# Kernel tuning notes

Hardware: AMD Instinct MI355X
Metric: run time of the kernel (lower is better)

## Reference

```python
import jax, jax.numpy as jnp
import numpy as np
import math

D_MODEL = 512
N_HEADS = 8
D_FF = 2048
TOP_FACTOR = 5
LN_EPS = 1e-5


def _layernorm(x, g, b):
    m = jnp.mean(x, axis=-1, keepdims=True)
    v = jnp.mean((x - m) ** 2, axis=-1, keepdims=True)
    return (x - m) / jnp.sqrt(v + LN_EPS) * g + b


def _prob_sparse_attn(q_in, k_in, v_in, wq, bq, wk, bk, wv, bv, wo, bo):
    # weights stored (in, out): y = x @ w + b  (equivalent to torch Linear)
    B, Lq, dm = q_in.shape
    Lk = k_in.shape[1]
    H, D = N_HEADS, dm // N_HEADS
    q = (q_in @ wq + bq).reshape(B, Lq, H, D).transpose(0, 2, 1, 3)  # (B,H,Lq,D)
    k = (k_in @ wk + bk).reshape(B, Lk, H, D).transpose(0, 2, 1, 3)
    v = (v_in @ wv + bv).reshape(B, Lk, H, D).transpose(0, 2, 1, 3)

    qn = q / jnp.linalg.norm(q, axis=-1, keepdims=True)
    kn = k / jnp.linalg.norm(k, axis=-1, keepdims=True)
    # full cosine-similarity matrix, reduced to a row mean (as in the original)
    scores_all = jnp.einsum('bhqd,bhkd->bhqk', qn, kn)
    mean_scores = scores_all.mean(axis=-1)  # (B,H,Lq)

    u = max(1, Lq // TOP_FACTOR)
    _, top_idx = jax.lax.top_k(mean_scores, u)  # (B,H,u)

    q_sel = jnp.take_along_axis(q, top_idx[..., None], axis=2)  # (B,H,u,D)
    scores = jnp.einsum('bhud,bhkd->bhuk', q_sel, k) / math.sqrt(D)
    attn = jax.nn.softmax(scores, axis=-1)
    ctx_sel = jnp.einsum('bhuk,bhkd->bhud', attn, v)  # (B,H,u,D)

    b_ix = jnp.arange(B)[:, None, None]
    h_ix = jnp.arange(H)[None, :, None]
    context = jnp.zeros((B, H, Lq, D), dtype=q.dtype).at[b_ix, h_ix, top_idx].set(ctx_sel)
    out = context.transpose(0, 2, 1, 3).reshape(B, Lq, dm)
    return out @ wo + bo


def _decoder_layer(x, enc_out, p):
    xn = _layernorm(x, p['ln1_g'], p['ln1_b'])
    x = x + _prob_sparse_attn(xn, xn, xn, p['sa_wq'], p['sa_bq'], p['sa_wk'], p['sa_bk'],
                              p['sa_wv'], p['sa_bv'], p['sa_wo'], p['sa_bo'])
    xn = _layernorm(x, p['ln2_g'], p['ln2_b'])
    x = x + _prob_sparse_attn(xn, enc_out, enc_out, p['ca_wq'], p['ca_bq'], p['ca_wk'], p['ca_bk'],
                              p['ca_wv'], p['ca_bv'], p['ca_wo'], p['ca_bo'])
    xn = _layernorm(x, p['ln3_g'], p['ln3_b'])
    h = jax.nn.relu(xn @ p['ff_w1'] + p['ff_b1'])
    return x + (h @ p['ff_w2'] + p['ff_b2'])


def setup_inputs() -> dict:
    key = jax.random.key(0)
    ks = iter(jax.random.split(key, 32))
    B, L = 2, 2048
    dm, dff = D_MODEL, D_FF
    s = 1.0 / math.sqrt(dm)
    inp = {
        'x': jax.random.normal(next(ks), (B, L, dm), jnp.float32),
        'enc_out': jax.random.normal(next(ks), (B, L, dm), jnp.float32),
    }
    for pre in ('sa', 'ca'):
        for nm in ('wq', 'wk', 'wv', 'wo'):
            inp[f'{pre}_{nm}'] = jax.random.normal(next(ks), (dm, dm), jnp.float32) * s
            inp[f'{pre}_{nm[1:] and "b" + nm[1:]}'] = jnp.zeros((dm,), jnp.float32)
    inp['ff_w1'] = jax.random.normal(next(ks), (dm, dff), jnp.float32) * s
    inp['ff_b1'] = jnp.zeros((dff,), jnp.float32)
    inp['ff_w2'] = jax.random.normal(next(ks), (dff, dm), jnp.float32) / math.sqrt(dff)
    inp['ff_b2'] = jnp.zeros((dm,), jnp.float32)
    for i in (1, 2, 3):
        inp[f'ln{i}_g'] = jnp.ones((dm,), jnp.float32)
        inp[f'ln{i}_b'] = jnp.zeros((dm,), jnp.float32)
    return inp


def reference(x, enc_out,
              sa_wq, sa_bq, sa_wk, sa_bk, sa_wv, sa_bv, sa_wo, sa_bo,
              ca_wq, ca_bq, ca_wk, ca_bk, ca_wv, ca_bv, ca_wo, ca_bo,
              ff_w1, ff_b1, ff_w2, ff_b2,
              ln1_g, ln1_b, ln2_g, ln2_b, ln3_g, ln3_b):
    p = dict(sa_wq=sa_wq, sa_bq=sa_bq, sa_wk=sa_wk, sa_bk=sa_bk, sa_wv=sa_wv, sa_bv=sa_bv,
             sa_wo=sa_wo, sa_bo=sa_bo, ca_wq=ca_wq, ca_bq=ca_bq, ca_wk=ca_wk, ca_bk=ca_bk,
             ca_wv=ca_wv, ca_bv=ca_bv, ca_wo=ca_wo, ca_bo=ca_bo,
             ff_w1=ff_w1, ff_b1=ff_b1, ff_w2=ff_w2, ff_b2=ff_b2,
             ln1_g=ln1_g, ln1_b=ln1_b, ln2_g=ln2_g, ln2_b=ln2_b, ln3_g=ln3_g, ln3_b=ln3_b)
    return _decoder_layer(x, enc_out, p)
```

## Files before the change

### kernel.cpp

```cpp
#include <hip/hip_runtime.h>

#define BB 2
#define LL 2048
#define DM 512
#define NH 8
#define DH 64
#define DFF 2048
#define UU 409
#define ROWS (BB*LL)
#define X_ELEMS 2097152
#define NCHUNK 8

typedef unsigned short u16;
typedef __attribute__((ext_vector_type(8))) short short8;
typedef __attribute__((ext_vector_type(4))) float floatx4;

#define G_TOTAL 38200000
__device__ float g_buf[G_TOTAL];
__device__ int   g_isbf16;

#define A_Q     10495488
#define A_K     12592640
#define A_V     14689792
#define A_MKN   25175552
#define A_MS    25176576
#define A_RANK  25209344
#define A_PARTK 25242112
#define A_LIST  25274880
#define A_PO    25281536
#define A_PML   29475840
#define A_CTXF  16786944
#define XN_H    16796672
#define XN_L    18893824
#define CTX_H   33573888
#define CTX_L   35671040
#define ENC_H   37768192
#define ENC_L   39865344
#define AH_H    41962496
#define KH16    59213824
#define KL16    61310976
#define VTH16   63408128
#define VTL16   65505280
#define WT_SAQKV 67864576
#define WT_SAO   69437440
#define WT_CAQ   69961728
#define WT_CAKV  70486016
#define WT_CAO   71534592
#define WT_W1    72058880
#define WT_W2    74156032

__constant__ int c_end[28] = {
    2097152, 4194304, 4456448, 4456960, 4719104, 4719616, 4981760, 4982272,
    5244416, 5244928, 5507072, 5507584, 5769728, 5770240, 6032384, 6032896,
    6295040, 6295552, 7344128, 7346176, 8394752, 8395264, 8395776, 8396288,
    8396800, 8397312, 8397824, 8398336
};
__constant__ int sm_idx[16] = {3,5,7,9,11,13,15,17,19,21,22,23,24,25,26,27};
__constant__ int sm_cum[16] = {64,128,192,256,320,384,448,512,768,832,896,960,1024,1088,1152,1216};
#define XG 262144
#define EG 262144
#define SG 1216

__device__ __forceinline__ float bf2f(u16 x) {
    union { unsigned int u; float f; } c; c.u = ((unsigned int)x) << 16; return c.f;
}
__device__ __forceinline__ u16 f2bf(float f) {
    union { float f; unsigned int u; } c; c.f = f;
    unsigned int u = c.u;
    return (u16)((u + 0x7FFFu + ((u >> 16) & 1u)) >> 16);
}
__device__ __forceinline__ unsigned cvtpk_bf16(float a, float b) {
    unsigned r;
    asm("v_cvt_pk_bf16_f32 %0, %1, %2" : "=v"(r) : "v"(a), "v"(b));
    return r;
}

struct P28 { const void* p[28]; };
struct I3 { int v[3]; };

__constant__ int tj[10][6] = {
    {2,  WT_SAQKV, 0,    512,  786432, 8},
    {4,  WT_SAQKV, 512,  512,  786432, 8},
    {6,  WT_SAQKV, 1024, 512,  786432, 8},
    {8,  WT_SAO,   0,    512,  262144, 8},
    {10, WT_CAQ,   0,    512,  262144, 8},
    {12, WT_CAKV,  0,    512,  524288, 8},
    {14, WT_CAKV,  512,  512,  524288, 8},
    {16, WT_CAO,   0,    512,  262144, 8},
    {18, WT_W1,    0,    512, 1048576, 32},
    {20, WT_W2,    0,   2048, 1048576, 8},
};
__constant__ int tcum[10] = {64, 128, 192, 256, 320, 384, 448, 512, 768, 1024};
__global__ void prep_all(P28 ps) {
    const int f = (((const u16*)ps.p[22])[0] == 0x3F80u) ? 1 : 0;
    if (blockIdx.x == 0 && threadIdx.x == 0) g_isbf16 = f;
    u16* gb16 = (u16*)g_buf;
    if (blockIdx.x < 1024) {
        int bid = blockIdx.x;
        int j = 0;
        while (bid >= tcum[j]) j++;
        int t = bid - (j ? tcum[j - 1] : 0);
        int widx = tj[j][0], wt = tj[j][1], col0 = tj[j][2];
        int K = tj[j][3], lo = tj[j][4], txn = tj[j][5];
        int Nsrc = txn * 64;
        int n0 = (t % txn) * 64, k0 = (t / txn) * 64;
        __shared__ float tb[64][65];
        int c = threadIdx.x & 63, r0 = threadIdx.x >> 6;
        const void* W = ps.p[widx];
        u16* WTh = gb16 + wt;
        for (int i = 0; i < 16; i++) {
            int r = r0 + 4 * i;
            size_t src = (size_t)(k0 + r) * Nsrc + n0 + c;
            tb[r][c] = f ? bf2f(((const u16*)W)[src]) : ((const float*)W)[src];
        }
        __syncthreads();
        for (int i = 0; i < 16; i++) {
            int r = r0 + 4 * i;
            float v = tb[c][r];
            u16 hi = f2bf(v);
            size_t o = (size_t)(col0 + n0 + r) * K + k0 + c;
            WTh[o] = hi;
            WTh[lo + o] = f2bf(v - bf2f(hi));
        }
        return;
    }
    int stride = 2048 * blockDim.x;
    for (int g = (blockIdx.x - 1024) * blockDim.x + threadIdx.x; g < XG + EG + SG; g += stride) {
        if (g < XG) {
            int e = g * 8;
            if (f) {
                uint4 raw = ((const uint4*)ps.p[0])[g];
                const u16* rr = (const u16*)&raw;
                float v[8] __attribute__((aligned(16)));
#pragma unroll
                for (int i = 0; i < 8; i++) v[i] = bf2f(rr[i]);
                *(float4*)(g_buf + e) = ((const float4*)v)[0];
                *(float4*)(g_buf + e + 4) = ((const float4*)v)[1];
            } else {
                *(uint4*)(g_buf + e)     = ((const uint4*)ps.p[0])[g * 2];
                *(uint4*)(g_buf + e + 4) = ((const uint4*)ps.p[0])[g * 2 + 1];
            }
        } else if (g < XG + EG) {
            int gl = g - XG;
            int e = gl * 8;
            float v[8] __attribute__((aligned(16)));
            if (f) {
                uint4 raw = ((const uint4*)ps.p[1])[gl];
                const u16* rr = (const u16*)&raw;
#pragma unroll
                for (int i = 0; i < 8; i++) v[i] = bf2f(rr[i]);
            } else {
                *(float4*)(v)     = ((const float4*)ps.p[1])[gl * 2];
                *(float4*)(v + 4) = ((const float4*)ps.p[1])[gl * 2 + 1];
            }
            u16 hh[8] __attribute__((aligned(16)));
            u16 lo[8] __attribute__((aligned(16)));
#pragma unroll
            for (int i = 0; i < 8; i++) { u16 hi = f2bf(v[i]); hh[i] = hi; lo[i] = f2bf(v[i] - bf2f(hi)); }
            *(uint4*)(&gb16[ENC_H + e]) = *(const uint4*)hh;
            *(uint4*)(&gb16[ENC_L + e]) = *(const uint4*)lo;
        } else {
            int t = g - XG - EG;
            int si = 0;
            while (t >= sm_cum[si]) si++;
            int s = sm_idx[si];
            int gl = t - (si ? sm_cum[si - 1] : 0);
            int e = gl * 8;
            float* dst = g_buf + c_end[s - 1] + e;
            if (f) {
                uint4 raw = *(const uint4*)((const u16*)ps.p[s] + e);
                const u16* rr = (const u16*)&raw;
#pragma unroll
                for (int i = 0; i < 8; i++) dst[i] = bf2f(rr[i]);
            } else {
                *(uint4*)(dst)     = *(const uint4*)((const float*)ps.p[s] + e);
                *(uint4*)(dst + 4) = *(const uint4*)((const float*)ps.p[s] + e + 4);
            }
        }
    }
}

__global__ void lnorm_k(int x_off, int g_off, int b_off, int yh_u16, int yl_u16) {
    int row = blockIdx.x;
    int tid = threadIdx.x;
    const float* x = g_buf + x_off + (size_t)row * DM;
    float a = x[tid], c = x[tid + 256];
    float s1 = a + c, s2 = a * a + c * c;
    for (int o = 32; o > 0; o >>= 1) { s1 += __shfl_xor(s1, o); s2 += __shfl_xor(s2, o); }
    __shared__ float r1[4], r2[4];
    int wave = tid >> 6, lane = tid & 63;
    if (lane == 0) { r1[wave] = s1; r2[wave] = s2; }
    __syncthreads();
    s1 = r1[0] + r1[1] + r1[2] + r1[3];
    s2 = r2[0] + r2[1] + r2[2] + r2[3];
    float mean = s1 * (1.0f / DM);
    float var  = s2 * (1.0f / DM) - mean * mean;
    float rstd = rsqrtf(var + 1e-5f);
    const float* gg = g_buf + g_off;
    const float* bb = g_buf + b_off;
    u16* yh = ((u16*)g_buf) + yh_u16 + (size_t)row * DM;
    u16* yl = ((u16*)g_buf) + yl_u16 + (size_t)row * DM;
    float v1 = (a - mean) * rstd * gg[tid]       + bb[tid];
    float v2 = (c - mean) * rstd * gg[tid + 256] + bb[tid + 256];
    u16 h1 = f2bf(v1), h2 = f2bf(v2);
    yh[tid] = h1;       yl[tid] = f2bf(v1 - bf2f(h1));
    yh[tid + 256] = h2; yl[tid + 256] = f2bf(v2 - bf2f(h2));
}

template<int WM, bool SPLIT, bool SEC, bool RELU, bool RESID, bool FINAL, bool OUTH>
__global__ void mgemm_k(I3 a_offs, I3 splt, I3 alz, int wt_u16_off, I3 boffs, int resid_off,
                        int out_off, void* __restrict__ dext, int M, int N, int K) {
    constexpr int BT_M = WM * 32;
    constexpr int A4 = BT_M * 4;
    __shared__ u16 Ash[BT_M * 40];
    __shared__ u16 Asl[SPLIT ? BT_M * 40 : 8];
    __shared__ u16 Bsh[128 * 40];
    __shared__ u16 Bsl[SPLIT ? 128 * 40 : 8];
    int ntb = blockIdx.y;
    int sec_blk = SEC ? ((ntb * 128) >> 9) : 0;
    const u16* Ah = ((const u16*)g_buf) + a_offs.v[sec_blk];
    const u16* Al = Ah + (size_t)M * K;
    const u16* WTh = ((const u16*)g_buf) + wt_u16_off;
    const u16* WTl = WTh + (size_t)N * K;
    const int isbf = g_isbf16;
    const bool use_al = SPLIT && splt.v[sec_blk] && !(alz.v[sec_blk] && isbf);
    const bool use_bl = SPLIT && splt.v[sec_blk] && !isbf;
    int tid = threadIdx.x;
    int lane = tid & 63, wid = tid >> 6;
    int wm = wid >> 1, wn = wid & 1;
    int quad = lane >> 4, l15 = lane & 15;
    int m0 = blockIdx.x * BT_M, n0 = ntb * 128;
    floatx4 acc[WM][4];
#pragma unroll
    for (int i = 0; i < WM; i++)
#pragma unroll
        for (int j = 0; j < 4; j++) acc[i][j] = (floatx4){0.f, 0.f, 0.f, 0.f};
    for (int k0 = 0; k0 < K; k0 += 32) {
#pragma unroll
        for (int i = 0; i < (A4 + 255) / 256; i++) {
            int idx8 = tid + 256 * i;
            if (A4 % 256 == 0 || idx8 < A4) {
                int r = idx8 >> 2, c8 = (idx8 & 3) * 8;
                *(uint4*)(&Ash[r * 40 + c8]) = *(const uint4*)(Ah + (size_t)(m0 + r) * K + k0 + c8);
                if (SPLIT && use_al)
                    *(uint4*)(&Asl[r * 40 + c8]) = *(const uint4*)(Al + (size_t)(m0 + r) * K + k0 + c8);
            }
        }
#pragma unroll
        for (int i = 0; i < 2; i++) {
            int idx8 = tid + 256 * i;
            int r = idx8 >> 2, c8 = (idx8 & 3) * 8;
            *(uint4*)(&Bsh[r * 40 + c8]) = *(const uint4*)(WTh + (size_t)(n0 + r) * K + k0 + c8);
            if (SPLIT && use_bl)
                *(uint4*)(&Bsl[r * 40 + c8]) = *(const uint4*)(WTl + (size_t)(n0 + r) * K + k0 + c8);
        }
        __syncthreads();
        short8 ah[WM], bh[4], al[WM], bl[4];
#pragma unroll
        for (int i = 0; i < WM; i++) {
            int ro = (wm * WM * 16 + i * 16 + l15) * 40 + quad * 8;
            ah[i] = *(const short8*)(&Ash[ro]);
            if (SPLIT && use_al) al[i] = *(const short8*)(&Asl[ro]);
        }
#pragma unroll
        for (int j = 0; j < 4; j++) {
            int ro = (wn * 64 + j * 16 + l15) * 40 + quad * 8;
            bh[j] = *(const short8*)(&Bsh[ro]);
            if (SPLIT && use_bl) bl[j] = *(const short8*)(&Bsl[ro]);
        }
#pragma unroll
        for (int i = 0; i < WM; i++)
#pragma unroll
            for (int j = 0; j < 4; j++) {
                acc[i][j] = __builtin_amdgcn_mfma_f32_16x16x32_bf16(ah[i], bh[j], acc[i][j], 0, 0, 0);
                if constexpr (SPLIT) {
                    if (use_bl)
                        acc[i][j] = __builtin_amdgcn_mfma_f32_16x16x32_bf16(ah[i], bl[j], acc[i][j], 0, 0, 0);
                    if (use_al)
                        acc[i][j] = __builtin_amdgcn_mfma_f32_16x16x32_bf16(al[i], bh[j], acc[i][j], 0, 0, 0);
                }
            }
        __syncthreads();
    }
#pragma unroll
    for (int i = 0; i < WM; i++)
#pragma unroll
        for (int j = 0; j < 4; j++)
#pragma unroll
            for (int r = 0; r < 4; r++) {
                int row = m0 + wm * WM * 16 + i * 16 + quad * 4 + r;
                int col = n0 + wn * 64 + j * 16 + l15;
                int sec = SEC ? (col >> 9) : 0;
                int ci  = SEC ? (col & 511) : col;
                float v = acc[i][j][r] + g_buf[boffs.v[sec] + ci];
                if (RELU) v = fmaxf(v, 0.f);
                if (RESID) v += g_buf[resid_off + (size_t)row * N + col];
                if (FINAL) {
                    if (g_isbf16) ((u16*)dext)[(size_t)row * N + col] = f2bf(v);
                    else          ((float*)dext)[(size_t)row * N + col] = v;
                } else if (OUTH) {
                    ((u16*)g_buf)[out_off + (size_t)row * N + col] = f2bf(v);
                } else if (SEC) {
                    g_buf[out_off + ((size_t)sec * ROWS + row) * 512 + ci] = v;
                } else {
                    g_buf[out_off + (size_t)row * N + col] = v;
                }
            }
}

template<bool SPLIT, bool RESID, bool FINAL>
__global__ __launch_bounds__(64) void sgemm_k(int a_off, int sp, int alz, int wt_u16_off,
        int b_off, int resid_off, int out_off, void* __restrict__ dext, int M, int N, int K) {
    const u16* gb = (const u16*)g_buf;
    const u16* Ah = gb + a_off;
    const u16* Alp = Ah + (size_t)M * K;
    const u16* Bh = gb + wt_u16_off;
    const u16* Blp = Bh + (size_t)N * K;
    const int isbf = g_isbf16;
    const bool ual = SPLIT && sp && !(alz && isbf);
    const bool ubl = SPLIT && sp && !isbf;
    int mtiles = M >> 4;
    int bid = blockIdx.x;
    int mt = bid % mtiles, nt = bid / mtiles;
    int n0 = nt * 64, m0 = mt * 16;
    int lane = threadIdx.x;
    int quad = lane >> 4, l15 = lane & 15;
    const u16* ap  = Ah  + (size_t)(m0 + l15) * K + quad * 8;
    const u16* alq = Alp + (size_t)(m0 + l15) * K + quad * 8;
    const u16* bp  = Bh  + (size_t)(n0 + l15) * K + quad * 8;
    const u16* blq = Blp + (size_t)(n0 + l15) * K + quad * 8;
    floatx4 acc[4];
#pragma unroll
    for (int j = 0; j < 4; j++) acc[j] = (floatx4){0.f, 0.f, 0.f, 0.f};

    short8 AH0, AH1, AH2, AH3, AL0, AL1, AL2, AL3;
    short8 BH0[4], BH1[4], BH2[4], BH3[4], BL0[4], BL1[4], BL2[4], BL3[4];

#define SLOAD(P, KK) do { int kk_ = (KK); \
        AH##P = *(const short8*)(ap + kk_); \
        if (ual) AL##P = *(const short8*)(alq + kk_); \
        _Pragma("unroll") \
        for (int j = 0; j < 4; j++) { \
            BH##P[j] = *(const short8*)(bp + (size_t)j * 16 * K + kk_); \
            if (ubl) BL##P[j] = *(const short8*)(blq + (size_t)j * 16 * K + kk_); \
        } } while (0)

#define SMFMA(P) do { \
        _Pragma("unroll") \
        for (int j = 0; j < 4; j++) { \
            acc[j] = __builtin_amdgcn_mfma_f32_16x16x32_bf16(AH##P, BH##P[j], acc[j], 0, 0, 0); \
            if (SPLIT) { \
                if (ubl) acc[j] = __builtin_amdgcn_mfma_f32_16x16x32_bf16(AH##P, BL##P[j], acc[j], 0, 0, 0); \
                if (ual) acc[j] = __builtin_amdgcn_mfma_f32_16x16x32_bf16(AL##P, BH##P[j], acc[j], 0, 0, 0); \
            } \
        } } while (0)

    SLOAD(0, 0); SLOAD(1, 32); SLOAD(2, 64); SLOAD(3, 96);
    int k0 = 0;
    for (; k0 + 128 < K; k0 += 128) {
        SMFMA(0); SLOAD(0, k0 + 128);
        SMFMA(1); SLOAD(1, k0 + 160);
        SMFMA(2); SLOAD(2, k0 + 192);
        SMFMA(3); SLOAD(3, k0 + 224);
    }
    SMFMA(0); SMFMA(1); SMFMA(2); SMFMA(3);
#undef SLOAD
#undef SMFMA

    const float* bias = g_buf + b_off;
#pragma unroll
    for (int j = 0; j < 4; j++)
#pragma unroll
        for (int r = 0; r < 4; r++) {
            int row = m0 + quad * 4 + r;
            int col = n0 + j * 16 + l15;
            float v = acc[j][r] + bias[col];
            if (RESID) v += g_buf[resid_off + (size_t)row * N + col];
            if (FINAL) {
                if (isbf) ((u16*)dext)[(size_t)row * N + col] = f2bf(v);
                else      ((float*)dext)[(size_t)row * N + col] = v;
            } else {
                g_buf[out_off + (size_t)row * N + col] = v;
            }
        }
}

__global__ void meankn_p1(int k_off, int part_off) {
    int bh = blockIdx.x >> 5, chunk = blockIdx.x & 31;
    int b = bh >> 3, h = bh & 7;
    int wave = threadIdx.x >> 6, lane = threadIdx.x & 63;
    const float* base = g_buf + k_off + (size_t)b * LL * DM + (size_t)h * DH + lane;
    float acc = 0.f;
    for (int t = 0; t < 16; t++) {
        int j = chunk * 64 + wave * 16 + t;
        float kv = base[(size_t)j * DM];
        float s = kv * kv;
        for (int o = 32; o > 0; o >>= 1) s += __shfl_xor(s, o);
        acc += kv / sqrtf(fmaxf(s, 1e-30f));
    }
    __shared__ float red[4][64];
    red[wave][lane] = acc;
    __syncthreads();
    if (threadIdx.x < 64)
        g_buf[part_off + (size_t)blockIdx.x * 64 + threadIdx.x] =
            red[0][threadIdx.x] + red[1][threadIdx.x] + red[2][threadIdx.x] + red[3][threadIdx.x];
}

__global__ void mscore_k(int q_off, int part_off, int ms_off) {
    int bh = blockIdx.y, b = bh >> 3, h = bh & 7;
    int tid = threadIdx.x;
    __shared__ float mk[64];
    if (tid < 64) {
        float s = 0.f;
        for (int c = 0; c < 32; c++) s += g_buf[part_off + (size_t)(bh * 32 + c) * 64 + tid];
        mk[tid] = s * (1.0f / LL);
    }
    __syncthreads();
    int w = tid >> 6, lane = tid & 63;
    float m = mk[lane];
#pragma unroll
    for (int it = 0; it < 8; it++) {
        int row = blockIdx.x * 32 + it * 4 + w;
        float qv = g_buf[q_off + ((size_t)b * LL + row) * DM + h * DH + lane];
        float s = qv * qv, d = qv * m;
        for (int o = 32; o > 0; o >>= 1) { s += __shfl_xor(s, o); d += __shfl_xor(d, o); }
        if (lane == 0) g_buf[ms_off + bh * LL + row] = d / sqrtf(fmaxf(s, 1e-30f));
    }
}

__global__ void topsel_k(int ms_off, int list_off, int rank_off, int u) {
    __shared__ float s[LL];
    int bh = blockIdx.y, chunk = blockIdx.x;
    for (int i = threadIdx.x; i < LL; i += 256) s[i] = g_buf[ms_off + bh * LL + i];
    __syncthreads();
    int il = threadIdx.x >> 2;
    int i = chunk * 64 + il;
    int jq = threadIdx.x & 3;
    float si = s[i];
    int cnt = 0;
    for (int t = 0; t < 512; t++) {
        int j = jq * 512 + t;
        float sj = s[j];
        cnt += (sj > si) || (sj == si && j < i);
    }
    cnt += __shfl_xor(cnt, 1);
    cnt += __shfl_xor(cnt, 2);
    if (jq == 0) {
        int* list = (int*)(g_buf + list_off);
        int* rank = (int*)(g_buf + rank_off);
        if (cnt < u) { list[bh * 416 + cnt] = i; rank[bh * LL + i] = cnt; }
        else rank[bh * LL + i] = -1;
    }
}

template<bool LO>
__global__ void kvprep_k(int k_off, int v_off) {
    int bh = blockIdx.y, b = bh >> 3, h = bh & 7;
    int tok0 = blockIdx.x * 64;
    int tid = threadIdx.x;
    __shared__ float vt[64][68];
    u16* gb16 = (u16*)g_buf;
    int tok = tid >> 2, dq = (tid & 3) * 16;
    const float* kp = g_buf + k_off + ((size_t)(b * LL + tok0 + tok)) * DM + h * DH + dq;
    const float* vp = g_buf + v_off + ((size_t)(b * LL + tok0 + tok)) * DM + h * DH + dq;
    float kv[16] __attribute__((aligned(16)));
#pragma unroll
    for (int i = 0; i < 4; i++) *(float4*)(kv + 4 * i) = *(const float4*)(kp + 4 * i);
    u16 hh[16] __attribute__((aligned(16)));
    u16 lo[16] __attribute__((aligned(16)));
#pragma unroll
    for (int i = 0; i < 16; i++) { hh[i] = f2bf(kv[i]); if (LO) lo[i] = f2bf(kv[i] - bf2f(hh[i])); }
    size_t ko = ((size_t)(bh * LL + tok0 + tok)) * DH + dq;
    *(uint4*)(gb16 + KH16 + ko)     = ((const uint4*)hh)[0];
    *(uint4*)(gb16 + KH16 + ko + 8) = ((const uint4*)hh)[1];
    if (LO) {
        *(uint4*)(gb16 + KL16 + ko)     = ((const uint4*)lo)[0];
        *(uint4*)(gb16 + KL16 + ko + 8) = ((const uint4*)lo)[1];
    }
#pragma unroll
    for (int i = 0; i < 4; i++) *(float4*)(&vt[tok][dq + 4 * i]) = *(const float4*)(vp + 4 * i);
    __syncthreads();
    int d = tid >> 2, tq = (tid & 3) * 16;
    float vv[16];
#pragma unroll
    for (int i = 0; i < 16; i++) vv[i] = vt[tq + i][d];
#pragma unroll
    for (int i = 0; i < 16; i++) { hh[i] = f2bf(vv[i]); if (LO) lo[i] = f2bf(vv[i] - bf2f(hh[i])); }
    size_t vo = ((size_t)(bh * DH + d)) * LL + tok0 + tq;
    *(uint4*)(gb16 + VTH16 + vo)     = ((const uint4*)hh)[0];
    *(uint4*)(gb16 + VTH16 + vo + 8) = ((const uint4*)hh)[1];
    if (LO) {
        *(uint4*)(gb16 + VTL16 + vo)     = ((const uint4*)lo)[0];
        *(uint4*)(gb16 + VTL16 + vo + 8) = ((const uint4*)lo)[1];
    }
}

template<bool S3>
__global__ __launch_bounds__(256, 4) void attn_flash(int q_off, int kh_off, int kl_off,
        int vth_off, int vtl_off, int list_off, int po_off, int pml_off, int u) {
    int bid = blockIdx.x;
    int grp = bid & 127;
    int sxt = bid >> 7;
    int bh = grp & 15, chunk = grp >> 4;
    int b = bh >> 3, h = bh & 7;
    int tid = threadIdx.x, lane = tid & 63, w = tid >> 6;
    int quad = lane >> 4, l15 = lane & 15;
    const int* list = (const int*)(g_buf + list_off);

    short8 qh[2], ql[2];
    {
        int slot_q = sxt * 64 + w * 16 + l15;
        int qidx = list[bh * 416 + (slot_q < u ? slot_q : u - 1)];
        const float* qp = g_buf + q_off + ((size_t)b * LL + qidx) * DM + h * DH;
#pragma unroll
        for (int d2 = 0; d2 < 2; d2++) {
            float v[8] __attribute__((aligned(16)));
            *(float4*)(v)     = *(const float4*)(qp + d2 * 32 + quad * 8);
            *(float4*)(v + 4) = *(const float4*)(qp + d2 * 32 + quad * 8 + 4);
            u16 hh[8] __attribute__((aligned(16)));
            u16 lo[8] __attribute__((aligned(16)));
#pragma unroll
            for (int j = 0; j < 8; j++) {
                float s = v[j] * 0.125f;
                u16 hi = f2bf(s); hh[j] = hi; lo[j] = f2bf(s - bf2f(hi));
            }
            qh[d2] = *(const short8*)hh; ql[d2] = *(const short8*)lo;
        }
    }

    __shared__ u16 Ksh[32 * 68];
    __shared__ u16 Ksl[S3 ? 32 * 68 : 8];
    __shared__ u16 Vth[64 * 36];
    __shared__ u16 Vtl[S3 ? 64 * 36 : 8];

    const u16* gb16 = (const u16*)g_buf;
    const u16* KHp = gb16 + kh_off + (size_t)bh * LL * DH;
    const u16* KLp = gb16 + kl_off + (size_t)bh * LL * DH;
    const u16* VHp = gb16 + vth_off + (size_t)bh * DH * LL;
    const u16* VLp = gb16 + vtl_off + (size_t)bh * DH * LL;
    int krow = tid >> 3, kcol = (tid & 7) * 8;
    int vd = tid >> 2, vcol = (tid & 3) * 8;

    int aA = ((((lane >> 4) & 1) << 5) | l15) << 2;
    int aB = aA + 64;
    bool hiT = (quad >= 2);

    uint4 pre[S3 ? 4 : 2];
    auto issue = [&](int row0) {
        pre[0] = *(const uint4*)(KHp + (size_t)(row0 + krow) * DH + kcol);
        pre[1] = *(const uint4*)(VHp + (size_t)vd * LL + row0 + vcol);
        if constexpr (S3) {
            pre[2] = *(const uint4*)(KLp + (size_t)(row0 + krow) * DH + kcol);
            pre[3] = *(const uint4*)(VLp + (size_t)vd * LL + row0 + vcol);
        }
    };
    auto commit = [&]() {
        *(uint4*)(&Ksh[krow * 68 + kcol]) = pre[0];
        *(uint4*)(&Vth[vd * 36 + vcol]) = pre[1];
        if constexpr (S3) {
            *(uint4*)(&Ksl[krow * 68 + kcol]) = pre[2];
            *(uint4*)(&Vtl[vd * 36 + vcol]) = pre[3];
        }
    };

    float m_run = -3.0e38f, l_run = 0.f;
    floatx4 acc_o[4];
#pragma unroll
    for (int j = 0; j < 4; j++) acc_o[j] = (floatx4){0.f, 0.f, 0.f, 0.f};

    issue(chunk * 256);
    for (int kt = 0; kt < 8; ++kt) {
        __syncthreads();
        commit();
        if (kt < 7) issue(chunk * 256 + (kt + 1) * 32);
        __syncthreads();
        floatx4 sacc[2];
#pragma unroll
        for (int t = 0; t < 2; t++) {
            sacc[t] = (floatx4){0.f, 0.f, 0.f, 0.f};
#pragma unroll
            for (int d2 = 0; d2 < 2; d2++) {
                int ro = (t * 16 + l15) * 68 + d2 * 32 + quad * 8;
                short8 kh = *(const short8*)(&Ksh[ro]);
                sacc[t] = __builtin_amdgcn_mfma_f32_16x16x32_bf16(kh, qh[d2], sacc[t], 0, 0, 0);
                sacc[t] = __builtin_amdgcn_mfma_f32_16x16x32_bf16(kh, ql[d2], sacc[t], 0, 0, 0);
                if constexpr (S3) {
                    short8 kl = *(const short8*)(&Ksl[ro]);
                    sacc[t] = __builtin_amdgcn_mfma_f32_16x16x32_bf16(kl, qh[d2], sacc[t], 0, 0, 0);
                }
            }
        }
        float mx = fmaxf(fmaxf(fmaxf(sacc[0][0], sacc[0][1]), fmaxf(sacc[0][2], sacc[0][3])),
                         fmaxf(fmaxf(sacc[1][0], sacc[1][1]), fmaxf(sacc[1][2], sacc[1][3])));
        mx = fmaxf(mx, __shfl_xor(mx, 16));
        mx = fmaxf(mx, __shfl_xor(mx, 32));
        float mn = fmaxf(m_run, mx);
        float alpha = __expf(m_run - mn);
        m_run = mn;
#pragma unroll
        for (int t = 0; t < 2; t++)
#pragma unroll
            for (int r = 0; r < 4; r++) sacc[t][r] = __expf(sacc[t][r] - mn);
        float ls = (sacc[0][0] + sacc[0][1]) + (sacc[0][2] + sacc[0][3])
                 + (sacc[1][0] + sacc[1][1]) + (sacc[1][2] + sacc[1][3]);
        ls += __shfl_xor(ls, 16);
        ls += __shfl_xor(ls, 32);
        l_run = l_run * alpha + ls;
        unsigned phw[2][2], plw[2][2];
#pragma unroll
        for (int t = 0; t < 2; t++)
#pragma unroll
            for (int hh = 0; hh < 2; hh++) {
                float s0 = sacc[t][2 * hh], s1 = sacc[t][2 * hh + 1];
                unsigned hw = cvtpk_bf16(s0, s1);
                phw[t][hh] = hw;
                float r0 = s0 - __uint_as_float(hw << 16);
                float r1 = s1 - __uint_as_float(hw & 0xFFFF0000u);
                plw[t][hh] = cvtpk_bf16(r0, r1);
            }
        union { unsigned wd[4]; short8 v; } pbh, pbl;
#pragma unroll
        for (int hh = 0; hh < 2; hh++) {
            int a0 = __builtin_amdgcn_ds_bpermute(aA, (int)phw[0][hh]);
            int a1 = __builtin_amdgcn_ds_bpermute(aA, (int)phw[1][hh]);
            pbh.wd[hh] = (unsigned)(hiT ? a1 : a0);
            int b0 = __builtin_amdgcn_ds_bpermute(aB, (int)phw[0][hh]);
            int b1 = __builtin_amdgcn_ds_bpermute(aB, (int)phw[1][hh]);
            pbh.wd[2 + hh] = (unsigned)(hiT ? b1 : b0);
            int c0 = __builtin_amdgcn_ds_bpermute(aA, (int)plw[0][hh]);
            int c1 = __builtin_amdgcn_ds_bpermute(aA, (int)plw[1][hh]);
            pbl.wd[hh] = (unsigned)(hiT ? c1 : c0);
            int d0 = __builtin_amdgcn_ds_bpermute(aB, (int)plw[0][hh]);
            int d1 = __builtin_amdgcn_ds_bpermute(aB, (int)plw[1][hh]);
            pbl.wd[2 + hh] = (unsigned)(hiT ? d1 : d0);
        }
#pragma unroll
        for (int j = 0; j < 4; j++)
#pragma unroll
            for (int r = 0; r < 4; r++) acc_o[j][r] *= alpha;
#pragma unroll
        for (int j = 0; j < 4; j++) {
            int ro = (j * 16 + l15) * 36 + quad * 8;
            short8 vh = *(const short8*)(&Vth[ro]);
            acc_o[j] = __builtin_amdgcn_mfma_f32_16x16x32_bf16(vh, pbh.v, acc_o[j], 0, 0, 0);
            acc_o[j] = __builtin_amdgcn_mfma_f32_16x16x32_bf16(vh, pbl.v, acc_o[j], 0, 0, 0);
            if constexpr (S3) {
                short8 vl = *(const short8*)(&Vtl[ro]);
                acc_o[j] = __builtin_amdgcn_mfma_f32_16x16x32_bf16(vl, pbh.v, acc_o[j], 0, 0, 0);
            }
        }
    }
    int slot = sxt * 64 + w * 16 + l15;
    if (slot < u) {
        size_t rec = ((size_t)(bh * NCHUNK + chunk)) * 512 + slot;
        float* po = g_buf + po_off + rec * 64;
#pragma unroll
        for (int j = 0; j < 4; j++)
            *(float4*)(po + j * 16 + quad * 4) = *(const float4*)&acc_o[j];
        if (quad == 0) {
            float* pml = g_buf + pml_off + rec * 2;
            pml[0] = m_run; pml[1] = l_run;
        }
    }
}

__global__ void attn_combine(int po_off, int pml_off, int rank_off, int u) {
    int bh = blockIdx.y;
    int b = bh >> 3, h = bh & 7;
    int tid = threadIdx.x;
    int qi = tid >> 4;
    int kb = tid & 15;
    int ds = kb * 4;
    int row = blockIdx.x * 16 + qi;
    int rank = ((const int*)(g_buf + rank_off))[bh * LL + row];
    size_t idx = ((size_t)b * LL + row) * DM + h * DH + ds;
    if (rank < 0) {
        ushort4 z = {0, 0, 0, 0};
        *(ushort4*)(((u16*)g_buf) + CTX_H + idx) = z;
        *(ushort4*)(((u16*)g_buf) + CTX_L + idx) = z;
        return;
    }
    float m = -3.0e38f;
#pragma unroll
    for (int c = 0; c < NCHUNK; c++)
        m = fmaxf(m, g_buf[pml_off + (((size_t)(bh * NCHUNK + c)) * 512 + rank) * 2]);
    float l = 0.f, O0 = 0.f, O1 = 0.f, O2 = 0.f, O3 = 0.f;
#pragma unroll
    for (int c = 0; c < NCHUNK; c++) {
        size_t rec = ((size_t)(bh * NCHUNK + c)) * 512 + rank;
        const float* pml = g_buf + pml_off + rec * 2;
        float a = __expf(pml[0] - m);
        l += a * pml[1];
        float4 o = *(const float4*)(g_buf + po_off + rec * 64 + ds);
        O0 += a * o.x; O1 += a * o.y; O2 += a * o.z; O3 += a * o.w;
    }
    float inv = 1.0f / l;
    float o0 = O0 * inv, o1 = O1 * inv, o2 = O2 * inv, o3 = O3 * inv;
    ushort4 hv, lv;
    hv.x = f2bf(o0); lv.x = f2bf(o0 - bf2f(hv.x));
    hv.y = f2bf(o1); lv.y = f2bf(o1 - bf2f(hv.y));
    hv.z = f2bf(o2); lv.z = f2bf(o2 - bf2f(hv.z));
    hv.w = f2bf(o3); lv.w = f2bf(o3 - bf2f(hv.w));
    *(ushort4*)(((u16*)g_buf) + CTX_H + idx) = hv;
    *(ushort4*)(((u16*)g_buf) + CTX_L + idx) = lv;
}

extern "C" void kernel_launch(void* const* d_in, const int* in_sizes, int n_in,
                              void* d_out, int out_size, void* d_ws, size_t ws_size,
                              hipStream_t stream) {
    static const int SZ[28] = {
        2097152, 2097152,
        262144, 512, 262144, 512, 262144, 512, 262144, 512,
        262144, 512, 262144, 512, 262144, 512, 262144, 512,
        1048576, 2048, 1048576, 512,
        512, 512, 512, 512, 512, 512
    };
    int OFF[28];
    int cur = 0;
    for (int i = 0; i < 28; i++) { OFF[i] = cur; cur += SZ[i]; }

    P28 ps;
    for (int i = 0; i < 28; i++) ps.p[i] = d_in[i];
    prep_all<<<3072, 256, 0, stream>>>(ps);

    auto select_attend = [&](bool sa) {
        if (sa) kvprep_k<true><<<dim3(32, 16), 256, 0, stream>>>(A_K, A_V);
        else    kvprep_k<false><<<dim3(32, 16), 256, 0, stream>>>(A_K, A_V);
        meankn_p1<<<16 * 32, 256, 0, stream>>>(A_K, A_PARTK);
        mscore_k<<<dim3(64, 16), 256, 0, stream>>>(A_Q, A_PARTK, A_MS);
        topsel_k<<<dim3(32, 16), 256, 0, stream>>>(A_MS, A_LIST, A_RANK, UU);
        if (sa)
            attn_flash<true><<<896, 256, 0, stream>>>(
                A_Q, KH16, KL16, VTH16, VTL16, A_LIST, A_PO, A_PML, UU);
        else
            attn_flash<false><<<896, 256, 0, stream>>>(
                A_Q, KH16, KL16, VTH16, VTL16, A_LIST, A_PO, A_PML, UU);
        attn_combine<<<dim3(128, 16), 256, 0, stream>>>(A_PO, A_PML, A_RANK, UU);
    };

    lnorm_k<<<ROWS, 256, 0, stream>>>(OFF[0], OFF[22], OFF[23], XN_H, XN_L);
    mgemm_k<2, true, true, false, false, false, false><<<dim3(64, 12), 256, 0, stream>>>(
        I3{{XN_H, XN_H, XN_H}}, I3{{1, 1, 1}}, I3{{0, 0, 0}},
        WT_SAQKV, I3{{OFF[3], OFF[5], OFF[7]}}, 0, A_Q, nullptr, ROWS, 1536, 512);
    select_attend(true);
    sgemm_k<true, true, false><<<2048, 64, 0, stream>>>(
        CTX_H, 1, 0, WT_SAO, OFF[9], OFF[0], OFF[0], nullptr, ROWS, 512, 512);

    lnorm_k<<<ROWS, 256, 0, stream>>>(OFF[0], OFF[24], OFF[25], XN_H, XN_L);
    sgemm_k<true, false, false><<<2048, 64, 0, stream>>>(
        XN_H, 1, 0, WT_CAQ, OFF[11], 0, A_Q, nullptr, ROWS, 512, 512);
    mgemm_k<2, true, true, false, false, false, false><<<dim3(64, 8), 256, 0, stream>>>(
        I3{{ENC_H, ENC_H, ENC_H}}, I3{{1, 0, 0}}, I3{{1, 0, 0}},
        WT_CAKV, I3{{OFF[13], OFF[15], 0}}, 0, A_K, nullptr, ROWS, 1024, 512);
    select_attend(false);
    sgemm_k<false, true, false><<<2048, 64, 0, stream>>>(
        CTX_H, 0, 0, WT_CAO, OFF[17], OFF[0], OFF[0], nullptr, ROWS, 512, 512);

    lnorm_k<<<ROWS, 256, 0, stream>>>(OFF[0], OFF[26], OFF[27], XN_H, XN_L);
    mgemm_k<4, false, false, true, false, false, true><<<dim3(32, 16), 256, 0, stream>>>(
        I3{{XN_H, 0, 0}}, I3{{0, 0, 0}}, I3{{0, 0, 0}},
        WT_W1, I3{{OFF[19], 0, 0}}, 0, AH_H, nullptr, ROWS, 2048, 512);
    sgemm_k<false, true, true><<<2048, 64, 0, stream>>>(
        AH_H, 0, 0, WT_W2, OFF[21], OFF[0], 0, d_out, ROWS, 512, 2048);
}
```

Before: 621.0 us.

## Register-prefetch next K tile in mgemm and add sgemm launch bound hint

The tiled MFMA GEMM now loads the next K-slice from global memory into registers while the current slice is being computed, then writes it to shared memory at the top of the next iteration. This software pipelining is meant to hide global load latency behind the MFMA work, and the trailing barrier moves to the start of the loop. It also adds a min-blocks hint of 2 to the small sgemm kernel's launch bounds. The cost is extra registers for the prefetch buffers, which could reduce occupancy, especially in the split-precision variants.

```diff
diff --git a/kernel.cpp b/kernel.cpp
--- a/kernel.cpp
+++ b/kernel.cpp
@@ -212,6 +212,7 @@
                         int out_off, void* __restrict__ dext, int M, int N, int K) {
     constexpr int BT_M = WM * 32;
     constexpr int A4 = BT_M * 4;
+    constexpr int NA = (A4 + 255) / 256;
     __shared__ u16 Ash[BT_M * 40];
     __shared__ u16 Asl[SPLIT ? BT_M * 40 : 8];
     __shared__ u16 Bsh[128 * 40];
@@ -230,30 +231,58 @@
     int wm = wid >> 1, wn = wid & 1;
     int quad = lane >> 4, l15 = lane & 15;
     int m0 = blockIdx.x * BT_M, n0 = ntb * 128;
-    floatx4 acc[WM][4];
-#pragma unroll
-    for (int i = 0; i < WM; i++)
-#pragma unroll
-        for (int j = 0; j < 4; j++) acc[i][j] = (floatx4){0.f, 0.f, 0.f, 0.f};
-    for (int k0 = 0; k0 < K; k0 += 32) {
-#pragma unroll
-        for (int i = 0; i < (A4 + 255) / 256; i++) {
+
+    uint4 pA[NA], pAl[NA], pB[2], pBl[2];
+    auto issue = [&](int k0) {
+#pragma unroll
+        for (int i = 0; i < NA; i++) {
             int idx8 = tid + 256 * i;
             if (A4 % 256 == 0 || idx8 < A4) {
                 int r = idx8 >> 2, c8 = (idx8 & 3) * 8;
-                *(uint4*)(&Ash[r * 40 + c8]) = *(const uint4*)(Ah + (size_t)(m0 + r) * K + k0 + c8);
+                pA[i] = *(const uint4*)(Ah + (size_t)(m0 + r) * K + k0 + c8);
                 if (SPLIT && use_al)
-                    *(uint4*)(&Asl[r * 40 + c8]) = *(const uint4*)(Al + (size_t)(m0 + r) * K + k0 + c8);
+                    pAl[i] = *(const uint4*)(Al + (size_t)(m0 + r) * K + k0 + c8);
             }
         }
 #pragma unroll
         for (int i = 0; i < 2; i++) {
             int idx8 = tid + 256 * i;
             int r = idx8 >> 2, c8 = (idx8 & 3) * 8;
-            *(uint4*)(&Bsh[r * 40 + c8]) = *(const uint4*)(WTh + (size_t)(n0 + r) * K + k0 + c8);
+            pB[i] = *(const uint4*)(WTh + (size_t)(n0 + r) * K + k0 + c8);
             if (SPLIT && use_bl)
-                *(uint4*)(&Bsl[r * 40 + c8]) = *(const uint4*)(WTl + (size_t)(n0 + r) * K + k0 + c8);
-        }
+                pBl[i] = *(const uint4*)(WTl + (size_t)(n0 + r) * K + k0 + c8);
+        }
+    };
+    auto commit = [&]() {
+#pragma unroll
+        for (int i = 0; i < NA; i++) {
+            int idx8 = tid + 256 * i;
+            if (A4 % 256 == 0 || idx8 < A4) {
+                int r = idx8 >> 2, c8 = (idx8 & 3) * 8;
+                *(uint4*)(&Ash[r * 40 + c8]) = pA[i];
+                if (SPLIT && use_al) *(uint4*)(&Asl[r * 40 + c8]) = pAl[i];
+            }
+        }
+#pragma unroll
+        for (int i = 0; i < 2; i++) {
+            int idx8 = tid + 256 * i;
+            int r = idx8 >> 2, c8 = (idx8 & 3) * 8;
+            *(uint4*)(&Bsh[r * 40 + c8]) = pB[i];
+            if (SPLIT && use_bl) *(uint4*)(&Bsl[r * 40 + c8]) = pBl[i];
+        }
+    };
+
+    floatx4 acc[WM][4];
+#pragma unroll
+    for (int i = 0; i < WM; i++)
+#pragma unroll
+        for (int j = 0; j < 4; j++) acc[i][j] = (floatx4){0.f, 0.f, 0.f, 0.f};
+
+    issue(0);
+    for (int k0 = 0; k0 < K; k0 += 32) {
+        __syncthreads();
+        commit();
+        if (k0 + 32 < K) issue(k0 + 32);
         __syncthreads();
         short8 ah[WM], bh[4], al[WM], bl[4];
 #pragma unroll
@@ -280,7 +309,6 @@
                         acc[i][j] = __builtin_amdgcn_mfma_f32_16x16x32_bf16(al[i], bh[j], acc[i][j], 0, 0, 0);
                 }
             }
-        __syncthreads();
     }
 #pragma unroll
     for (int i = 0; i < WM; i++)
@@ -309,7 +337,7 @@
 }
 
 template<bool SPLIT, bool RESID, bool FINAL>
-__global__ __launch_bounds__(64) void sgemm_k(int a_off, int sp, int alz, int wt_u16_off,
+__global__ __launch_bounds__(64, 2) void sgemm_k(int a_off, int sp, int alz, int wt_u16_off,
         int b_off, int resid_off, int out_off, void* __restrict__ dext, int M, int N, int K) {
     const u16* gb = (const u16*)g_buf;
     const u16* Ah = gb + a_off;
```

After: 668.9 us. 7.7% more time.
